# Optimization experiments

Hardware: AMD Instinct MI355X
Metric: run time of the kernel (lower is better)

## Reference

```python
import jax, jax.numpy as jnp
import numpy as np

B, T, C = 2, 2048, 2048
NH, NKV = 16, 16
HD = C // NH            # 128
GATE_CH = 32
ROPE_BASE = 10000.0


def setup_inputs() -> dict:
    key = jax.random.key(0)
    ks = jax.random.split(key, 8)
    x = jax.random.normal(ks[0], (B, T, C), jnp.float32)
    ve = jax.random.normal(ks[1], (B, T, C), jnp.float32)
    # RoPE tables: half-dim rotation, shape broadcastable to [B, T, H, HD//2]
    d2 = HD // 2
    inv_freq = 1.0 / (ROPE_BASE ** (jnp.arange(d2, dtype=jnp.float32) / d2))
    angles = jnp.arange(T, dtype=jnp.float32)[:, None] * inv_freq[None, :]  # [T, d2]
    cos = jnp.cos(angles)[None, :, None, :]  # [1, T, 1, d2]
    sin = jnp.sin(angles)[None, :, None, :]
    s = 0.02
    Wq = jax.random.normal(ks[2], (C, NH * HD), jnp.float32) * s
    Wk = jax.random.normal(ks[3], (C, NKV * HD), jnp.float32) * s
    Wv = jax.random.normal(ks[4], (C, NKV * HD), jnp.float32) * s
    Wgate = jax.random.normal(ks[5], (GATE_CH, NKV), jnp.float32) * s
    Wproj = jax.random.normal(ks[6], (NH * HD, C), jnp.float32) * s
    return {"x": x, "ve": ve, "cos": cos, "sin": sin,
            "Wq": Wq, "Wk": Wk, "Wv": Wv, "Wgate": Wgate, "Wproj": Wproj}


def _apply_rotary(x, cos, sin):
    d = x.shape[3] // 2
    x1, x2 = x[..., :d], x[..., d:]
    return jnp.concatenate([x1 * cos + x2 * sin, x1 * -sin + x2 * cos], axis=3)


def _rms_norm(x):
    return x * jax.lax.rsqrt(jnp.mean(x * x, axis=-1, keepdims=True) + 1e-6)


def reference(x, ve, cos, sin, Wq, Wk, Wv, Wgate, Wproj):
    b, t, c = x.shape
    q = (x @ Wq).reshape(b, t, NH, HD)
    k = (x @ Wk).reshape(b, t, NKV, HD)
    v = (x @ Wv).reshape(b, t, NKV, HD)
    # value-embedding gate
    ve_r = ve.reshape(b, t, NKV, HD)
    gate = 2.0 * jax.nn.sigmoid(x[..., :GATE_CH] @ Wgate)  # [B, T, NKV]
    v = v + gate[..., None] * ve_r
    # RoPE then QK-RMSNorm
    q = _rms_norm(_apply_rotary(q, cos, sin))
    k = _rms_norm(_apply_rotary(k, cos, sin))
    # causal attention, scale = 1/sqrt(head_dim)
    scale = 1.0 / np.sqrt(HD).astype(np.float32)
    scores = jnp.einsum('bqhd,bkhd->bhqk', q, k) * scale
    causal = jnp.tril(jnp.ones((t, t), dtype=bool))
    scores = jnp.where(causal, scores, jnp.finfo(scores.dtype).min)
    probs = jax.nn.softmax(scores, axis=-1)
    y = jnp.einsum('bhqk,bkhd->bqhd', probs, v)
    y = y.reshape(b, t, NH * HD)
    return y @ Wproj
```

## Files before the change

kernel.cpp:

```cpp
#include <hip/hip_runtime.h>
#include <stdint.h>

typedef short bf16x8 __attribute__((ext_vector_type(8)));
typedef float f32x4 __attribute__((ext_vector_type(4)));

#define ASYNC16(g, l) __builtin_amdgcn_global_load_lds( \
    (const __attribute__((address_space(1))) unsigned int*)(g), \
    (__attribute__((address_space(3))) unsigned int*)(l), 16, 0, 0)

__device__ __forceinline__ float bf2f(short u) {
  union { unsigned int i; float f; } v;
  v.i = ((unsigned int)(unsigned short)u) << 16;
  return v.f;
}
__device__ __forceinline__ short f2bf(float f) {
  union { float f; unsigned int i; } v;
  v.f = f;
  return (short)(unsigned short)((v.i + 0x8000u) >> 16);
}
__device__ __forceinline__ float ldf(const void* p, long i, int isbf) {
  return isbf ? bf2f(((const short*)p)[i]) : ((const float*)p)[i];
}

__global__ void detect_dtype(const short* __restrict__ x, int* __restrict__ flag) {
  if (threadIdx.x == 0 && blockIdx.x == 0) {
    int cnt = 0;
    for (int i = 0; i < 128; ++i) {
      int e = (((unsigned short)x[i]) >> 7) & 0xFF;
      if (e >= 110 && e <= 136) ++cnt;
    }
    *flag = (cnt >= 120) ? 1 : 0;
  }
}

__global__ __launch_bounds__(256) void convert_x(
    const void* __restrict__ xin, short* __restrict__ xb, const int* __restrict__ flag) {
  long i = (long)blockIdx.x * 2048 + (long)threadIdx.x * 8;
  if (*flag) {
    *(bf16x8*)(xb + i) = *(const bf16x8*)((const short*)xin + i);
  } else {
    const float* xf = (const float*)xin;
    short tmp[8];
    #pragma unroll
    for (int j = 0; j < 8; ++j) tmp[j] = f2bf(xf[i + j]);
    *(bf16x8*)(xb + i) = *(bf16x8*)tmp;
  }
}

__global__ __launch_bounds__(256) void transpose_w(
    const void* __restrict__ S0, short* __restrict__ D0,
    const void* __restrict__ S1, short* __restrict__ D1,
    const void* __restrict__ S2, short* __restrict__ D2,
    const int* __restrict__ flag)
{
  int z = blockIdx.z;
  const void* S = (z == 0) ? S0 : (z == 1) ? S1 : S2;
  short* D = (z == 0) ? D0 : (z == 1) ? D1 : D2;
  int isbf = *flag;
  __shared__ short tile[32][33];
  int c0 = blockIdx.x * 32, r0 = blockIdx.y * 32;
  int tx = threadIdx.x, ty = threadIdx.y;
  #pragma unroll
  for (int i = 0; i < 4; ++i)
    tile[ty + 8*i][tx] = f2bf(ldf(S, (long)(r0 + ty + 8*i) * 2048 + c0 + tx, isbf));
  __syncthreads();
  #pragma unroll
  for (int i = 0; i < 4; ++i)
    D[(long)(c0 + ty + 8*i) * 2048 + r0 + tx] = tile[tx][ty + 8*i];
}

__global__ __launch_bounds__(256) void transpose_v(
    const short* __restrict__ Vr, short* __restrict__ Vt)
{
  __shared__ short tile[32][33];
  int bh = blockIdx.z;
  int b = bh >> 4, h = bh & 15;
  int t0 = blockIdx.x * 32, d0 = blockIdx.y * 32;
  int tx = threadIdx.x, ty = threadIdx.y;
  #pragma unroll
  for (int i = 0; i < 4; ++i)
    tile[ty + 8*i][tx] = Vr[(long)(b*2048 + t0 + ty + 8*i) * 2048 + h*128 + d0 + tx];
  __syncthreads();
  #pragma unroll
  for (int i = 0; i < 4; ++i)
    Vt[((long)bh * 128 + d0 + ty + 8*i) * 2048 + t0 + tx] = tile[tx][ty + 8*i];
}

template<typename OutT>
__global__ __launch_bounds__(256) void gemm_bt(
    const short* __restrict__ A,
    const short* __restrict__ B0, const short* __restrict__ B1, const short* __restrict__ B2,
    OutT* __restrict__ C0, OutT* __restrict__ C1, OutT* __restrict__ C2,
    int M, int N, int K)
{
  int z = blockIdx.z;
  const short* Bt = (z == 0) ? B0 : (z == 1) ? B1 : B2;
  OutT* C = (z == 0) ? C0 : (z == 1) ? C1 : C2;

  int m0 = blockIdx.y * 128, n0 = blockIdx.x * 128;
  int tid = threadIdx.x;
  int lane = tid & 63, w = tid >> 6;
  int quad = lane >> 4, l16 = lane & 15;
  int wm = w >> 1, wn = w & 1;

  __shared__ short As[128][64];
  __shared__ short Bs[128][64];

  f32x4 zero4 = {0.f, 0.f, 0.f, 0.f};
  f32x4 acc[4][4];
  #pragma unroll
  for (int i = 0; i < 4; ++i)
    #pragma unroll
    for (int j = 0; j < 4; ++j) acc[i][j] = zero4;

  int r8 = lane >> 3;
  int srow = w * 32 + r8;
  int scol = ((lane & 7) ^ r8) * 8;

  for (int k0 = 0; k0 < K; k0 += 64) {
    #pragma unroll
    for (int i = 0; i < 4; ++i) {
      ASYNC16(A  + (long)(m0 + srow + i*8) * K + k0 + scol, &As[w*32 + i*8][0]);
      ASYNC16(Bt + (long)(n0 + srow + i*8) * K + k0 + scol, &Bs[w*32 + i*8][0]);
    }
    __syncthreads();
    #pragma unroll
    for (int kt = 0; kt < 2; ++kt) {
      int po = ((kt*4 + quad) ^ (l16 & 7)) * 8;
      bf16x8 af[4], bfr[4];
      #pragma unroll
      for (int i = 0; i < 4; ++i)
        af[i] = *(const bf16x8*)&As[wm*64 + i*16 + l16][po];
      #pragma unroll
      for (int j = 0; j < 4; ++j)
        bfr[j] = *(const bf16x8*)&Bs[wn*64 + j*16 + l16][po];
      #pragma unroll
      for (int i = 0; i < 4; ++i)
        #pragma unroll
        for (int j = 0; j < 4; ++j)
          acc[i][j] = __builtin_amdgcn_mfma_f32_16x16x32_bf16(af[i], bfr[j], acc[i][j], 0, 0, 0);
    }
    __syncthreads();
  }

  #pragma unroll
  for (int i = 0; i < 4; ++i)
    #pragma unroll
    for (int j = 0; j < 4; ++j) {
      int row = m0 + wm*64 + i*16 + quad*4;
      int col = n0 + wn*64 + j*16 + l16;
      #pragma unroll
      for (int r = 0; r < 4; ++r) {
        float v = acc[i][j][r];
        if constexpr (sizeof(OutT) == 4)
          C[(long)(row + r) * N + col] = v;
        else
          C[(long)(row + r) * N + col] = (OutT)f2bf(v);
      }
    }
}

__global__ __launch_bounds__(256) void pointwise(
    const short* __restrict__ xb, const void* __restrict__ ve,
    const void* __restrict__ cosb, const void* __restrict__ sinb,
    const void* __restrict__ Wg, const int* __restrict__ flag,
    short* __restrict__ Qr, short* __restrict__ Kr, short* __restrict__ Vr)
{
  int row = blockIdx.x;
  int tid = threadIdx.x;
  int isbf = *flag;
  __shared__ float xg[32];
  __shared__ float gates[16];
  if (tid < 32) xg[tid] = bf2f(xb[(long)row * 2048 + tid]);
  __syncthreads();
  if (tid < 16) {
    float g = 0.f;
    #pragma unroll
    for (int i = 0; i < 32; ++i) g += xg[i] * ldf(Wg, i*16 + tid, isbf);
    gates[tid] = 2.0f / (1.0f + __expf(-g));
  }
  __syncthreads();
  #pragma unroll
  for (int it = 0; it < 8; ++it) {
    int idx = it * 256 + tid;
    int h = idx >> 7;
    long p = (long)row * 2048 + idx;
    Vr[p] = f2bf(bf2f(Vr[p]) + gates[h] * ldf(ve, p, isbf));
  }
  int lane = tid & 63, w = tid >> 6;
  int t = row & 2047;
  #pragma unroll
  for (int it = 0; it < 8; ++it) {
    int unit = it * 4 + w;
    short* P = (unit < 16) ? Qr : Kr;
    int h = unit & 15;
    long base = (long)row * 2048 + h * 128;
    float x1 = bf2f(P[base + lane]);
    float x2 = bf2f(P[base + lane + 64]);
    float c = ldf(cosb, t*64 + lane, isbf);
    float s = ldf(sinb, t*64 + lane, isbf);
    float r1 = x1 * c + x2 * s;
    float r2 = -x1 * s + x2 * c;
    float ss = r1*r1 + r2*r2;
    #pragma unroll
    for (int off = 32; off; off >>= 1) ss += __shfl_xor(ss, off);
    float rn = rsqrtf(ss * (1.0f/128.0f) + 1e-6f);
    P[base + lane]      = f2bf(r1 * rn);
    P[base + lane + 64] = f2bf(r2 * rn);
  }
}

#define FL_C1 0.12751741f
#define FL_C2 16.321698f

__global__ __launch_bounds__(256) void flash(
    const short* __restrict__ Q, const short* __restrict__ K,
    const short* __restrict__ Vt, short* __restrict__ Y)
{
  int bx = blockIdx.x;
  int bh = blockIdx.y;
  int b = bh >> 4, h = bh & 15;
  int tid = threadIdx.x;
  int lane = tid & 63, w = tid >> 6;
  int quad = lane >> 4, l16 = lane & 15;

  __shared__ short Ks[2][64*128];
  __shared__ short Vts[2][128*64];
  __shared__ short Ps[4][16*72];

  int qtA = bx, qtB = 31 - bx;
  int nA = qtA + 1, nB = qtB + 1;
  int total = nA + nB;

  int kkey = tid >> 4;
  int klo  = (tid & 15) ^ (kkey & 7);
  int vd   = tid >> 3;
  int vlo  = (tid & 7) ^ (vd & 7);
  const short* Kbase = K + (long)(b*2048 + kkey) * 2048 + h*128 + klo*8;
  const short* Vbase = Vt + ((long)bh*128 + vd) * 2048 + vlo*8;

  f32x4 zero4 = {0.f, 0.f, 0.f, 0.f};
  f32x4 o[8];
  float l_i[4];
  bf16x8 qf[4];
  bf16x8 ones;
  #pragma unroll
  for (int j = 0; j < 8; ++j) ones[j] = (short)0x3F80;

  auto stage = [&](int tt, int buf) {
    int tl = (tt < nA) ? tt : tt - nA;
    long ko = (long)tl * 64 * 2048;
    int  vo = tl * 64;
    #pragma unroll
    for (int i = 0; i < 4; ++i)
      ASYNC16(Kbase + ko + (long)i*16*2048, &Ks[buf][(i*16 + w*4)*128]);
    #pragma unroll
    for (int i = 0; i < 4; ++i)
      ASYNC16(Vbase + vo + (long)i*32*2048, &Vts[buf][(i*32 + w*8)*64]);
  };
  auto loadQ = [&](int qt) {
    const short* Qb = Q + (long)(b*2048 + qt*64 + w*16 + l16) * 2048 + h*128;
    #pragma unroll
    for (int kt = 0; kt < 4; ++kt)
      qf[kt] = *(const bf16x8*)(Qb + kt*32 + quad*8);
  };
  auto flushO = [&](int qt) {
    #pragma unroll
    for (int r = 0; r < 4; ++r) {
      float inv = 1.0f / fmaxf(l_i[r], 1e-30f);
      short* yp = Y + (long)(b*2048 + qt*64 + w*16 + quad*4 + r) * 2048 + h*128;
      #pragma unroll
      for (int c8 = 0; c8 < 8; ++c8)
        yp[c8*16 + l16] = f2bf(o[c8][r] * inv);
    }
  };

  #pragma unroll
  for (int c = 0; c < 8; ++c) o[c] = zero4;
  #pragma unroll
  for (int r = 0; r < 4; ++r) l_i[r] = 0.f;
  loadQ(qtA);
  stage(0, 0);

  int qt = qtA, n_seg = nA, segbase = 0;
  for (int tt = 0; tt < total; ++tt) {
    int buf = tt & 1;
    asm volatile("s_waitcnt vmcnt(0)" ::: "memory");
    __builtin_amdgcn_s_barrier();
    if (tt + 1 < total) stage(tt + 1, buf ^ 1);
    if (tt == nA) {
      flushO(qtA);
      loadQ(qtB);
      #pragma unroll
      for (int c = 0; c < 8; ++c) o[c] = zero4;
      #pragma unroll
      for (int r = 0; r < 4; ++r) l_i[r] = 0.f;
      qt = qtB; n_seg = nB; segbase = nA;
    }
    int tloc = tt - segbase;
    int kv0 = tloc * 64;

    f32x4 s[4];
    #pragma unroll
    for (int c = 0; c < 4; ++c) {
      f32x4 acc = zero4;
      #pragma unroll
      for (int kt = 0; kt < 4; ++kt) {
        int po = ((kt*4 + quad) ^ (l16 & 7)) * 8;
        bf16x8 kf = *(const bf16x8*)&Ks[buf][(c*16 + l16)*128 + po];
        acc = __builtin_amdgcn_mfma_f32_16x16x32_bf16(qf[kt], kf, acc, 0, 0, 0);
      }
      s[c] = acc;
    }

    bool domask = (tloc == n_seg - 1);
    int qgb = qt*64 + w*16 + quad*4;
    #pragma unroll
    for (int c = 0; c < 4; ++c) {
      int kg = kv0 + c*16 + l16;
      #pragma unroll
      for (int r = 0; r < 4; ++r) {
        float t = s[c][r] * FL_C1 - FL_C2;
        if (domask && kg > qgb + r) t = -1000.0f;
        float pv = exp2f(t);
        Ps[w][(quad*4 + r)*72 + c*16 + l16] = f2bf(pv);
      }
    }
    asm volatile("s_waitcnt lgkmcnt(0)" ::: "memory");
    bf16x8 pa0 = *(const bf16x8*)&Ps[w][l16*72 + quad*8];
    bf16x8 pa1 = *(const bf16x8*)&Ps[w][l16*72 + 32 + quad*8];

    f32x4 racc = __builtin_amdgcn_mfma_f32_16x16x32_bf16(pa0, ones, zero4, 0, 0, 0);
    racc = __builtin_amdgcn_mfma_f32_16x16x32_bf16(pa1, ones, racc, 0, 0, 0);
    #pragma unroll
    for (int r = 0; r < 4; ++r) l_i[r] += racc[r];

    #pragma unroll
    for (int c8 = 0; c8 < 8; ++c8) {
      int po0 = ((0*4 + quad) ^ (l16 & 7)) * 8;
      int po1 = ((1*4 + quad) ^ (l16 & 7)) * 8;
      bf16x8 v0 = *(const bf16x8*)&Vts[buf][(c8*16 + l16)*64 + po0];
      bf16x8 v1 = *(const bf16x8*)&Vts[buf][(c8*16 + l16)*64 + po1];
      o[c8] = __builtin_amdgcn_mfma_f32_16x16x32_bf16(pa0, v0, o[c8], 0, 0, 0);
      o[c8] = __builtin_amdgcn_mfma_f32_16x16x32_bf16(pa1, v1, o[c8], 0, 0, 0);
    }
  }
  flushO(qtB);
}

extern "C" void kernel_launch(void* const* d_in, const int* in_sizes, int n_in,
                              void* d_out, int out_size, void* d_ws, size_t ws_size,
                              hipStream_t stream) {
  const void* x    = d_in[0];
  const void* ve   = d_in[1];
  const void* cosb = d_in[2];
  const void* sinb = d_in[3];
  const void* Wq   = d_in[4];
  const void* Wk   = d_in[5];
  const void* Wv   = d_in[6];
  const void* Wg   = d_in[7];
  const void* Wp   = d_in[8];
  float* out = (float*)d_out;

  int*   flag = (int*)d_ws;
  short* base = (short*)d_ws + 256;
  short* wt0 = base;
  short* wtk = base + 4194304L;
  short* wtv = base + 8388608L;
  short* Vt  = base + 4194304L;
  short* xb  = base + 12582912L;
  short* Y   = base + 12582912L;
  short* Qr  = base + 20971520L;
  short* Kr  = base + 29360128L;
  short* Vr  = base + 37748736L;

  detect_dtype<<<1, 64, 0, stream>>>((const short*)x, flag);
  convert_x<<<4096, 256, 0, stream>>>(x, xb, flag);
  transpose_w<<<dim3(64, 64, 3), dim3(32, 8), 0, stream>>>(Wq, wt0, Wk, wtk, Wv, wtv, flag);
  gemm_bt<short><<<dim3(16, 32, 3), 256, 0, stream>>>(xb, wt0, wtk, wtv, Qr, Kr, Vr, 4096, 2048, 2048);
  transpose_w<<<dim3(64, 64, 1), dim3(32, 8), 0, stream>>>(Wp, wt0, Wp, wt0, Wp, wt0, flag);
  pointwise<<<dim3(4096), 256, 0, stream>>>(xb, ve, cosb, sinb, Wg, flag, Qr, Kr, Vr);
  transpose_v<<<dim3(64, 4, 32), dim3(32, 8), 0, stream>>>(Vr, Vt);
  flash<<<dim3(16, 32), 256, 0, stream>>>(Qr, Kr, Vt, Y);
  gemm_bt<float><<<dim3(16, 32, 1), 256, 0, stream>>>(Y, wt0, wt0, wt0, out, out, out, 4096, 2048, 2048);
}
```

Baseline: 476.9 us.

## Triple-buffer GEMM with 512-thread 128x256 tiles and interleaved prefetch

Rewrites the bf16 GEMM to use 512-thread blocks computing 128x256 tiles, with a three-stage LDS ring buffer. Global-to-LDS async loads for tile t+2 are split across the two k-halves and interleaved with the MFMA phases. s_setprio is raised around the MFMA bursts in both the GEMM and the flash-attention kernel. The aim is to hide load latency and raise matrix-core utilisation, at the cost of more LDS per block (about 144KB) and extra barriers.

New measurement: 466.3 us. 2.2% less time.

```diff
diff --git a/kernel.cpp b/kernel.cpp
--- a/kernel.cpp
+++ b/kernel.cpp
@@ -87,7 +87,7 @@
 }
 
 template<typename OutT>
-__global__ __launch_bounds__(256) void gemm_bt(
+__global__ __launch_bounds__(512, 2) void gemm_bt(
     const short* __restrict__ A,
     const short* __restrict__ B0, const short* __restrict__ B1, const short* __restrict__ B2,
     OutT* __restrict__ C0, OutT* __restrict__ C1, OutT* __restrict__ C2,
@@ -97,14 +97,14 @@
   const short* Bt = (z == 0) ? B0 : (z == 1) ? B1 : B2;
   OutT* C = (z == 0) ? C0 : (z == 1) ? C1 : C2;
 
-  int m0 = blockIdx.y * 128, n0 = blockIdx.x * 128;
+  int m0 = blockIdx.y * 128, n0 = blockIdx.x * 256;
   int tid = threadIdx.x;
   int lane = tid & 63, w = tid >> 6;
   int quad = lane >> 4, l16 = lane & 15;
-  int wm = w >> 1, wn = w & 1;
-
-  __shared__ short As[128][64];
-  __shared__ short Bs[128][64];
+  int wm = w >> 2, wn = w & 3;
+
+  __shared__ short As[3][128*64];
+  __shared__ short Bs[3][256*64];
 
   f32x4 zero4 = {0.f, 0.f, 0.f, 0.f};
   f32x4 acc[4][4];
@@ -114,33 +114,80 @@
     for (int j = 0; j < 4; ++j) acc[i][j] = zero4;
 
   int r8 = lane >> 3;
-  int srow = w * 32 + r8;
-  int scol = ((lane & 7) ^ r8) * 8;
-
-  for (int k0 = 0; k0 < K; k0 += 64) {
-    #pragma unroll
-    for (int i = 0; i < 4; ++i) {
-      ASYNC16(A  + (long)(m0 + srow + i*8) * K + k0 + scol, &As[w*32 + i*8][0]);
-      ASYNC16(Bt + (long)(n0 + srow + i*8) * K + k0 + scol, &Bs[w*32 + i*8][0]);
-    }
-    __syncthreads();
-    #pragma unroll
-    for (int kt = 0; kt < 2; ++kt) {
-      int po = ((kt*4 + quad) ^ (l16 & 7)) * 8;
-      bf16x8 af[4], bfr[4];
-      #pragma unroll
-      for (int i = 0; i < 4; ++i)
-        af[i] = *(const bf16x8*)&As[wm*64 + i*16 + l16][po];
+  int oct = (lane & 7) ^ r8;
+  const short* Ab = A  + (long)(m0 + w*16 + r8) * K + oct*8;
+  const short* Bb = Bt + (long)(n0 + w*32 + r8) * K + oct*8;
+
+  int NT = K >> 6;
+
+  #pragma unroll
+  for (int u = 0; u < 2; ++u) ASYNC16(Ab + (long)u*8*K,      &As[0][(w*16 + u*8)*64]);
+  #pragma unroll
+  for (int u = 0; u < 4; ++u) ASYNC16(Bb + (long)u*8*K,      &Bs[0][(w*32 + u*8)*64]);
+  #pragma unroll
+  for (int u = 0; u < 2; ++u) ASYNC16(Ab + 64 + (long)u*8*K, &As[1][(w*16 + u*8)*64]);
+  #pragma unroll
+  for (int u = 0; u < 4; ++u) ASYNC16(Bb + 64 + (long)u*8*K, &Bs[1][(w*32 + u*8)*64]);
+  asm volatile("s_waitcnt vmcnt(6)" ::: "memory");
+  __builtin_amdgcn_s_barrier();
+
+  int buf = 0, sbuf = 2;
+  int po0 = ((0*4 + quad) ^ (l16 & 7)) * 8;
+  int po1 = ((1*4 + quad) ^ (l16 & 7)) * 8;
+
+  for (int t = 0; t < NT; ++t) {
+    long ks = (long)(t + 2) * 64;
+    bool st = (t + 2 < NT);
+
+    bf16x8 a0[4], b0[4];
+    #pragma unroll
+    for (int i = 0; i < 4; ++i)
+      a0[i] = *(const bf16x8*)&As[buf][(wm*64 + i*16 + l16)*64 + po0];
+    #pragma unroll
+    for (int j = 0; j < 4; ++j)
+      b0[j] = *(const bf16x8*)&Bs[buf][(wn*64 + j*16 + l16)*64 + po0];
+    if (st) {
+      #pragma unroll
+      for (int u = 0; u < 2; ++u) ASYNC16(Ab + ks + (long)u*8*K, &As[sbuf][(w*16 + u*8)*64]);
+      #pragma unroll
+      for (int u = 0; u < 2; ++u) ASYNC16(Bb + ks + (long)u*8*K, &Bs[sbuf][(w*32 + u*8)*64]);
+    }
+    __builtin_amdgcn_s_barrier();
+    __builtin_amdgcn_s_setprio(1);
+    #pragma unroll
+    for (int i = 0; i < 4; ++i)
       #pragma unroll
       for (int j = 0; j < 4; ++j)
-        bfr[j] = *(const bf16x8*)&Bs[wn*64 + j*16 + l16][po];
-      #pragma unroll
-      for (int i = 0; i < 4; ++i)
-        #pragma unroll
-        for (int j = 0; j < 4; ++j)
-          acc[i][j] = __builtin_amdgcn_mfma_f32_16x16x32_bf16(af[i], bfr[j], acc[i][j], 0, 0, 0);
-    }
-    __syncthreads();
+        acc[i][j] = __builtin_amdgcn_mfma_f32_16x16x32_bf16(a0[i], b0[j], acc[i][j], 0, 0, 0);
+    __builtin_amdgcn_s_setprio(0);
+    __builtin_amdgcn_s_barrier();
+
+    bf16x8 a1[4], b1[4];
+    #pragma unroll
+    for (int i = 0; i < 4; ++i)
+      a1[i] = *(const bf16x8*)&As[buf][(wm*64 + i*16 + l16)*64 + po1];
+    #pragma unroll
+    for (int j = 0; j < 4; ++j)
+      b1[j] = *(const bf16x8*)&Bs[buf][(wn*64 + j*16 + l16)*64 + po1];
+    if (st) {
+      #pragma unroll
+      for (int u = 2; u < 4; ++u) ASYNC16(Bb + ks + (long)u*8*K, &Bs[sbuf][(w*32 + u*8)*64]);
+    }
+    __builtin_amdgcn_s_barrier();
+    __builtin_amdgcn_s_setprio(1);
+    #pragma unroll
+    for (int i = 0; i < 4; ++i)
+      #pragma unroll
+      for (int j = 0; j < 4; ++j)
+        acc[i][j] = __builtin_amdgcn_mfma_f32_16x16x32_bf16(a1[i], b1[j], acc[i][j], 0, 0, 0);
+    __builtin_amdgcn_s_setprio(0);
+    if (t + 1 < NT) {
+      if (st) asm volatile("s_waitcnt vmcnt(6)" ::: "memory");
+      else    asm volatile("s_waitcnt vmcnt(0)" ::: "memory");
+      __builtin_amdgcn_s_barrier();
+    }
+    buf  = (buf  == 2) ? 0 : buf  + 1;
+    sbuf = (sbuf == 2) ? 0 : sbuf + 1;
   }
 
   #pragma unroll
@@ -247,16 +294,16 @@
   #pragma unroll
   for (int j = 0; j < 8; ++j) ones[j] = (short)0x3F80;
 
-  auto stage = [&](int tt, int buf) {
+  auto stage = [&](int tt, int bufp) {
     int tl = (tt < nA) ? tt : tt - nA;
     long ko = (long)tl * 64 * 2048;
     int  vo = tl * 64;
     #pragma unroll
     for (int i = 0; i < 4; ++i)
-      ASYNC16(Kbase + ko + (long)i*16*2048, &Ks[buf][(i*16 + w*4)*128]);
-    #pragma unroll
-    for (int i = 0; i < 4; ++i)
-      ASYNC16(Vbase + vo + (long)i*32*2048, &Vts[buf][(i*32 + w*8)*64]);
+      ASYNC16(Kbase + ko + (long)i*16*2048, &Ks[bufp][(i*16 + w*4)*128]);
+    #pragma unroll
+    for (int i = 0; i < 4; ++i)
+      ASYNC16(Vbase + vo + (long)i*32*2048, &Vts[bufp][(i*32 + w*8)*64]);
   };
   auto loadQ = [&](int qt) {
     const short* Qb = Q + (long)(b*2048 + qt*64 + w*16 + l16) * 2048 + h*128;
@@ -301,6 +348,7 @@
     int kv0 = tloc * 64;
 
     f32x4 s[4];
+    __builtin_amdgcn_s_setprio(1);
     #pragma unroll
     for (int c = 0; c < 4; ++c) {
       f32x4 acc = zero4;
@@ -312,6 +360,7 @@
       }
       s[c] = acc;
     }
+    __builtin_amdgcn_s_setprio(0);
 
     bool domask = (tloc == n_seg - 1);
     int qgb = qt*64 + w*16 + quad*4;
@@ -330,6 +379,7 @@
     bf16x8 pa0 = *(const bf16x8*)&Ps[w][l16*72 + quad*8];
     bf16x8 pa1 = *(const bf16x8*)&Ps[w][l16*72 + 32 + quad*8];
 
+    __builtin_amdgcn_s_setprio(1);
     f32x4 racc = __builtin_amdgcn_mfma_f32_16x16x32_bf16(pa0, ones, zero4, 0, 0, 0);
     racc = __builtin_amdgcn_mfma_f32_16x16x32_bf16(pa1, ones, racc, 0, 0, 0);
     #pragma unroll
@@ -344,6 +394,7 @@
       o[c8] = __builtin_amdgcn_mfma_f32_16x16x32_bf16(pa0, v0, o[c8], 0, 0, 0);
       o[c8] = __builtin_amdgcn_mfma_f32_16x16x32_bf16(pa1, v1, o[c8], 0, 0, 0);
     }
+    __builtin_amdgcn_s_setprio(0);
   }
   flushO(qtB);
 }
@@ -377,10 +428,10 @@
   detect_dtype<<<1, 64, 0, stream>>>((const short*)x, flag);
   convert_x<<<4096, 256, 0, stream>>>(x, xb, flag);
   transpose_w<<<dim3(64, 64, 3), dim3(32, 8), 0, stream>>>(Wq, wt0, Wk, wtk, Wv, wtv, flag);
-  gemm_bt<short><<<dim3(16, 32, 3), 256, 0, stream>>>(xb, wt0, wtk, wtv, Qr, Kr, Vr, 4096, 2048, 2048);
+  gemm_bt<short><<<dim3(8, 32, 3), 512, 0, stream>>>(xb, wt0, wtk, wtv, Qr, Kr, Vr, 4096, 2048, 2048);
   transpose_w<<<dim3(64, 64, 1), dim3(32, 8), 0, stream>>>(Wp, wt0, Wp, wt0, Wp, wt0, flag);
   pointwise<<<dim3(4096), 256, 0, stream>>>(xb, ve, cosb, sinb, Wg, flag, Qr, Kr, Vr);
   transpose_v<<<dim3(64, 4, 32), dim3(32, 8), 0, stream>>>(Vr, Vt);
   flash<<<dim3(16, 32), 256, 0, stream>>>(Qr, Kr, Vt, Y);
-  gemm_bt<float><<<dim3(16, 32, 1), 256, 0, stream>>>(Y, wt0, wt0, wt0, out, out, out, 4096, 2048, 2048);
-}
+  gemm_bt<float><<<dim3(8, 32, 1), 512, 0, stream>>>(Y, wt0, wt0, wt0, out, out, out, 4096, 2048, 2048);
+}
```
